# Kernel tuning notes

Measured on AMD Instinct MI355X. Metric: run time of the kernel, lower is better.

## Reference

```python
import jax, jax.numpy as jnp
import numpy as np

B, L1, L2, D = 32, 512, 512, 1024


def setup_inputs() -> dict:
    key = jax.random.key(0)
    k1, k2, k3, k4 = jax.random.split(key, 4)
    v1 = jax.random.normal(k1, (B, L1, D), dtype=jnp.float32)
    v2 = jax.random.normal(k2, (B, L2, D), dtype=jnp.float32)
    # row/column is fully masked (which would NaN the softmax).
    v1_mask = jax.random.uniform(k3, (B, L1)) < 0.2
    v2_mask = jax.random.uniform(k4, (B, L2)) < 0.2
    return {"v1": v1, "v2": v2, "v1_mask": v1_mask, "v2_mask": v2_mask}


def reference(v1, v2, v1_mask, v2_mask):
    # similarity: [B, L1, L2]
    sim = jnp.einsum("bid,bjd->bij", v1, v2)
    neg_inf = jnp.float32(-jnp.inf)
    # softmax over v2 positions (dim=2), masking padded v2 columns
    v1_v2_attn = jax.nn.softmax(
        jnp.where(v2_mask[:, None, :], neg_inf, sim), axis=2)
    # softmax over v1 positions (dim=1), masking padded v1 rows
    v2_v1_attn = jax.nn.softmax(
        jnp.where(v1_mask[:, :, None], neg_inf, sim), axis=1)
    attended_v1 = jnp.einsum("bij,bjd->bid", v1_v2_attn, v2)  # [B,L1,D]
    attended_v2 = jnp.einsum("bij,bid->bjd", v2_v1_attn, v1)  # [B,L2,D]
    attended_v1 = jnp.where(v1_mask[:, :, None], 0.0, attended_v1)
    attended_v2 = jnp.where(v2_mask[:, :, None], 0.0, attended_v2)
    return attended_v1, attended_v2
```

## Files before the change

kernel.cpp:

```cpp
#include <hip/hip_runtime.h>
#include <stdint.h>


#define Bn 32
#define Ln 512
#define Dn 1024

typedef __attribute__((ext_vector_type(4))) float f32x4;
typedef __attribute__((ext_vector_type(4))) unsigned short u16x4;
typedef __attribute__((ext_vector_type(8))) unsigned short u16x8;
typedef __attribute__((ext_vector_type(8))) __bf16 bf16x8;

__device__ __forceinline__ unsigned short f2bf(float f) {
  unsigned int u = __float_as_uint(f);
  u += 0x7FFFu + ((u >> 16) & 1u);
  return (unsigned short)(u >> 16);
}

__device__ __forceinline__ void async_cp16(const void* g, void* l) {
  __builtin_amdgcn_global_load_lds(
      (__attribute__((address_space(1))) void*)(g),
      (__attribute__((address_space(3))) void*)(l), 16, 0, 0);
}

__global__ __launch_bounds__(256) void conv_split(
    const float* __restrict__ v1, const float* __restrict__ v2,
    unsigned short* __restrict__ v1t, unsigned short* __restrict__ v2t,
    unsigned short* __restrict__ v1h, unsigned short* __restrict__ v1l,
    unsigned short* __restrict__ v2h, unsigned short* __restrict__ v2l) {
  __shared__ float tile[64][65];
  const int z = blockIdx.z;
  const float* src = (z < Bn) ? v1 : v2;
  unsigned short* dt = (z < Bn) ? v1t : v2t;
  unsigned short* dh = (z < Bn) ? v1h : v2h;
  unsigned short* dl = (z < Bn) ? v1l : v2l;
  const int b = z & 31;
  const int d0 = blockIdx.x << 6;
  const int l0 = blockIdx.y << 6;
  const int tid = threadIdx.x;
  const size_t bo = (size_t)b * Ln * Dn;

  f32x4 xa[2], xb[2];
#pragma unroll
  for (int it = 0; it < 2; it++) {
    int lin = (it << 8) + tid;
    int l = lin >> 3;
    int d8 = (lin & 7) << 3;
    const float* sp = src + (size_t)(b * Ln + l0 + l) * Dn + d0 + d8;
    xa[it] = *(const f32x4*)sp;
    xb[it] = *(const f32x4*)(sp + 4);
  }
#pragma unroll
  for (int it = 0; it < 2; it++) {
    int lin = (it << 8) + tid;
    int l = lin >> 3;
    int d8 = (lin & 7) << 3;
    float xs[8] = {xa[it][0], xa[it][1], xa[it][2], xa[it][3],
                   xb[it][0], xb[it][1], xb[it][2], xb[it][3]};
    u16x8 h8, lo8;
#pragma unroll
    for (int e = 0; e < 8; e++) {
      tile[l][d8 + e] = xs[e];
      unsigned int u = __float_as_uint(xs[e]);
      h8[e] = (unsigned short)(u >> 16);
      float hf = __uint_as_float(u & 0xFFFF0000u);
      lo8[e] = (unsigned short)(__float_as_uint(xs[e] - hf) >> 16);
    }
    int gl = l0 + l;
    int sd = (d0 + d8) ^ (((gl >> 1) & 3) << 3);
    size_t off = bo + (size_t)gl * Dn + sd;
    *(u16x8*)(dh + off) = h8;
    *(u16x8*)(dl + off) = lo8;
  }
  __syncthreads();
#pragma unroll
  for (int it = 0; it < 4; it++) {
    int lin = (it << 8) + tid;
    int d = lin >> 4;
    int l4 = (lin & 15) << 2;
    u16x4 o;
    o[0] = f2bf(tile[l4][d]);     o[1] = f2bf(tile[l4 + 1][d]);
    o[2] = f2bf(tile[l4 + 2][d]); o[3] = f2bf(tile[l4 + 3][d]);
    *(u16x4*)(dt + (size_t)(b * Dn + d0 + d) * Ln + l0 + l4) = o;
  }
}

__global__ __launch_bounds__(256) void sim_gemm(
    const unsigned short* __restrict__ Ahg, const unsigned short* __restrict__ Alg,
    const unsigned short* __restrict__ Bhg, const unsigned short* __restrict__ Blg,
    float* __restrict__ C, const int* __restrict__ v1m,
    const int* __restrict__ v2m,
    float* __restrict__ pmaxR, float* __restrict__ psumR,
    float* __restrict__ pmaxC, float* __restrict__ psumC) {
  __shared__ unsigned short sAh[2][4096], sAl[2][4096];
  __shared__ unsigned short sBh[2][4096], sBl[2][4096];
  const int bid = blockIdx.x;
  const int id = ((bid & 7) << 6) + (bid >> 3);
  const int b = id >> 4;
  const int m0 = ((id >> 2) & 3) << 7;
  const int n0 = (id & 3) << 7;
  const int tid = threadIdx.x;
  const int lane = tid & 63;
  const int wave = tid >> 6;
  const int wrow = (wave >> 1) << 6;
  const int wcol = (wave & 1) << 6;
  const int r = lane & 15;
  const int q = lane >> 4;
  const int srow = tid >> 2;
  const int skof = (tid & 3) << 3;
  const size_t bo = (size_t)b * Ln * Dn;
  const unsigned short* gah = Ahg + bo + (size_t)(m0 + srow) * Dn + skof;
  const unsigned short* gal = Alg + bo + (size_t)(m0 + srow) * Dn + skof;
  const unsigned short* gbh = Bhg + bo + (size_t)(n0 + srow) * Dn + skof;
  const unsigned short* gbl = Blg + bo + (size_t)(n0 + srow) * Dn + skof;
  const int ldsw = wave << 9;

#define SIM_STAGE(nb, kk)                                        \
  do {                                                           \
    async_cp16(gah + (kk), &sAh[nb][ldsw]);                      \
    async_cp16(gah + 64 * Dn + (kk), &sAh[nb][2048 + ldsw]);     \
    async_cp16(gal + (kk), &sAl[nb][ldsw]);                      \
    async_cp16(gal + 64 * Dn + (kk), &sAl[nb][2048 + ldsw]);     \
    async_cp16(gbh + (kk), &sBh[nb][ldsw]);                      \
    async_cp16(gbh + 64 * Dn + (kk), &sBh[nb][2048 + ldsw]);     \
    async_cp16(gbl + (kk), &sBl[nb][ldsw]);                      \
    async_cp16(gbl + 64 * Dn + (kk), &sBl[nb][2048 + ldsw]);     \
  } while (0)

  const f32x4 zero4 = {0.f, 0.f, 0.f, 0.f};
  f32x4 acc[4][4];
#pragma unroll
  for (int i = 0; i < 4; i++)
#pragma unroll
    for (int j = 0; j < 4; j++) acc[i][j] = zero4;

  SIM_STAGE(0, 0);
  __syncthreads();

  int cb = 0;
  for (int k0 = 0; k0 < Dn; k0 += 32, cb ^= 1) {
    if (k0 + 32 < Dn) SIM_STAGE(cb ^ 1, k0 + 32);
    bf16x8 ah[4], al[4], bh[4], bl[4];
#pragma unroll
    for (int t = 0; t < 4; t++) {
      int ra = wrow + (t << 4) + r;
      int sa = (ra << 5) + ((q ^ ((ra >> 1) & 3)) << 3);
      ah[t] = *(const bf16x8*)(&sAh[cb][sa]);
      al[t] = *(const bf16x8*)(&sAl[cb][sa]);
      int rb = wcol + (t << 4) + r;
      int sb = (rb << 5) + ((q ^ ((rb >> 1) & 3)) << 3);
      bh[t] = *(const bf16x8*)(&sBh[cb][sb]);
      bl[t] = *(const bf16x8*)(&sBl[cb][sb]);
    }
#pragma unroll
    for (int tm = 0; tm < 4; tm++)
#pragma unroll
      for (int tn = 0; tn < 4; tn++) {
        acc[tm][tn] = __builtin_amdgcn_mfma_f32_16x16x32_bf16(
            ah[tm], bh[tn], acc[tm][tn], 0, 0, 0);
        acc[tm][tn] = __builtin_amdgcn_mfma_f32_16x16x32_bf16(
            ah[tm], bl[tn], acc[tm][tn], 0, 0, 0);
        acc[tm][tn] = __builtin_amdgcn_mfma_f32_16x16x32_bf16(
            al[tm], bh[tn], acc[tm][tn], 0, 0, 0);
      }
    __syncthreads();
  }
#undef SIM_STAGE

  float* Cb = C + (size_t)b * Ln * Ln;
#pragma unroll
  for (int tm = 0; tm < 4; tm++) {
    int rowb = m0 + wrow + (tm << 4) + (q << 2);
#pragma unroll
    for (int reg = 0; reg < 4; reg++) {
      int row = rowb + reg;
#pragma unroll
      for (int tn = 0; tn < 4; tn++) {
        int col = n0 + wcol + (tn << 4) + r;
        Cb[(size_t)row * Ln + col] = acc[tm][tn][reg];
      }
    }
  }

  const int* mkr = v1m + (b << 9);
  const int* mkc = v2m + (b << 9);
  const float NEGINF = -__builtin_inff();
  unsigned cmb = 0;
#pragma unroll
  for (int tn = 0; tn < 4; tn++)
    cmb |= (mkc[n0 + wcol + (tn << 4) + r] ? 1u : 0u) << tn;
  unsigned rmb = 0;
#pragma unroll
  for (int t2 = 0; t2 < 16; t2++)
    rmb |= (mkr[m0 + wrow + ((t2 >> 2) << 4) + (q << 2) + (t2 & 3)] ? 1u : 0u)
           << t2;

  const int nsub = (n0 + wcol) >> 6;
#pragma unroll
  for (int tm = 0; tm < 4; tm++) {
#pragma unroll
    for (int reg = 0; reg < 4; reg++) {
      float m = NEGINF;
#pragma unroll
      for (int tn = 0; tn < 4; tn++)
        if (!((cmb >> tn) & 1)) m = fmaxf(m, acc[tm][tn][reg]);
#pragma unroll
      for (int off = 1; off < 16; off <<= 1)
        m = fmaxf(m, __shfl_xor(m, off));
      float s = 0.f;
#pragma unroll
      for (int tn = 0; tn < 4; tn++)
        if (!((cmb >> tn) & 1)) s += __expf(acc[tm][tn][reg] - m);
#pragma unroll
      for (int off = 1; off < 16; off <<= 1) s += __shfl_xor(s, off);
      if (r == 0) {
        int row = m0 + wrow + (tm << 4) + (q << 2) + reg;
        int idx = (((b << 3) + nsub) << 9) + row;
        pmaxR[idx] = m;
        psumR[idx] = s;
      }
    }
  }

  const int msub = (m0 + wrow) >> 6;
#pragma unroll
  for (int tn = 0; tn < 4; tn++) {
    float m = NEGINF;
#pragma unroll
    for (int tm = 0; tm < 4; tm++)
#pragma unroll
      for (int reg = 0; reg < 4; reg++)
        if (!((rmb >> ((tm << 2) + reg)) & 1))
          m = fmaxf(m, acc[tm][tn][reg]);
    m = fmaxf(m, __shfl_xor(m, 16));
    m = fmaxf(m, __shfl_xor(m, 32));
    float s = 0.f;
#pragma unroll
    for (int tm = 0; tm < 4; tm++)
#pragma unroll
      for (int reg = 0; reg < 4; reg++)
        if (!((rmb >> ((tm << 2) + reg)) & 1))
          s += __expf(acc[tm][tn][reg] - m);
    s += __shfl_xor(s, 16);
    s += __shfl_xor(s, 32);
    if (q == 0) {
      int col = n0 + wcol + (tn << 4) + r;
      int idx = (((b << 3) + msub) << 9) + col;
      pmaxC[idx] = m;
      psumC[idx] = s;
    }
  }
}

__global__ __launch_bounds__(256) void comb(
    const float* __restrict__ pmaxR, const float* __restrict__ psumR,
    const float* __restrict__ pmaxC, const float* __restrict__ psumC,
    float* __restrict__ rowmax, float* __restrict__ rowrs,
    float* __restrict__ colmax, float* __restrict__ colrs) {
  const int id = (blockIdx.x << 8) + threadIdx.x;
  const int side = id >> 14;
  const int x = id & 16383;
  const float* pm = side ? pmaxC : pmaxR;
  const float* ps = side ? psumC : psumR;
  const int bq = x >> 9;
  const int j = x & 511;
  const float NEGINF = -__builtin_inff();
  float mm[8], sv[8];
#pragma unroll
  for (int p = 0; p < 8; p++) {
    int idx = (((bq << 3) + p) << 9) + j;
    mm[p] = pm[idx];
    sv[p] = ps[idx];
  }
  float M = NEGINF;
#pragma unroll
  for (int p = 0; p < 8; p++) M = fmaxf(M, mm[p]);
  float S = 0.f;
#pragma unroll
  for (int p = 0; p < 8; p++)
    S += (mm[p] > NEGINF) ? sv[p] * __expf(mm[p] - M) : 0.f;
  float rs = 1.f / S;
  if (side) { colmax[x] = M; colrs[x] = rs; }
  else      { rowmax[x] = M; rowrs[x] = rs; }
}

__global__ __launch_bounds__(256) void norm_write(
    const float* __restrict__ sim, const int* __restrict__ v1m,
    const int* __restrict__ v2m,
    const float* __restrict__ rowmax, const float* __restrict__ rowrs,
    const float* __restrict__ colmax, const float* __restrict__ colrs,
    unsigned short* __restrict__ A1, unsigned short* __restrict__ A2t) {
  __shared__ unsigned short Tc[64][66];
  __shared__ float rm[64], rr[64], cmx[64], crx[64];
  __shared__ int jmk[64], imk[64];
  const int b = blockIdx.z;
  const int i0 = blockIdx.y << 6;
  const int j0 = blockIdx.x << 6;
  const int tid = threadIdx.x;
  if (tid < 64) {
    cmx[tid] = colmax[(b << 9) + j0 + tid];
    crx[tid] = colrs[(b << 9) + j0 + tid];
  } else if (tid < 128) {
    int t = tid - 64;
    rm[t] = rowmax[(b << 9) + i0 + t];
    rr[t] = rowrs[(b << 9) + i0 + t];
  } else if (tid < 192) {
    jmk[tid - 128] = v2m[(b << 9) + j0 + tid - 128];
  } else {
    imk[tid - 192] = v1m[(b << 9) + i0 + tid - 192];
  }
  __syncthreads();
  const int ri = tid >> 4;
  const int jj = (tid & 15) << 2;
  const float* Sb = sim + (size_t)b * (Ln * Ln);
  unsigned short* A1b = A1 + ((size_t)((b << 9) + i0)) * Ln + j0;
#pragma unroll
  for (int p = 0; p < 4; p++) {
    int il = (p << 4) + ri;
    f32x4 x = *(const f32x4*)(Sb + (size_t)(i0 + il) * Ln + j0 + jj);
    float rmv = rm[il], rrv = rr[il];
    int mrow = imk[il];
    u16x4 o1;
#pragma unroll
    for (int e = 0; e < 4; e++) {
      float e1 = jmk[jj + e] ? 0.f : __expf(x[e] - rmv) * rrv;
      o1[e] = f2bf(e1);
      float e2 = mrow ? 0.f : __expf(x[e] - cmx[jj + e]) * crx[jj + e];
      Tc[jj + e][il] = f2bf(e2);
    }
    *(u16x4*)(A1b + (size_t)il * Ln + jj) = o1;
  }
  __syncthreads();
  unsigned short* o = A2t + ((size_t)((b << 9) + j0)) * Ln + i0;
#pragma unroll
  for (int t = 0; t < 4; t++) {
    int c = (t << 8) + tid;
    int j = c >> 4;
    int ch = c & 15;
    u16x4 v;
    v[0] = Tc[j][(ch << 2)];     v[1] = Tc[j][(ch << 2) + 1];
    v[2] = Tc[j][(ch << 2) + 2]; v[3] = Tc[j][(ch << 2) + 3];
    *(u16x4*)(o + (size_t)j * Ln + (ch << 2)) = v;
  }
}

__global__ __launch_bounds__(256) void gemm_nt2(
    const unsigned short* __restrict__ A1g, const unsigned short* __restrict__ A2tg,
    const unsigned short* __restrict__ v2t, const unsigned short* __restrict__ v1t,
    float* __restrict__ out1, float* __restrict__ out2,
    const int* __restrict__ v1m, const int* __restrict__ v2m) {
  const int Mv = 512, Nv = 1024, Kv = 512;
  __shared__ unsigned short As[2][4096];
  __shared__ unsigned short Bs[2][4096];
  const int bid = blockIdx.x;
  const int id = ((bid & 7) << 8) + (bid >> 3);
  const int z = id >> 5;
  const int m0 = ((id >> 3) & 3) << 7;
  const int n0 = (id & 7) << 7;
  const int b = z & 31;
  const int w2 = z >> 5;
  const unsigned short* A = w2 ? A2tg : A1g;
  const unsigned short* Bm = w2 ? v1t : v2t;
  float* C = w2 ? out2 : out1;
  const int* rowmask = w2 ? v2m : v1m;
  const unsigned short* Ab = A + (size_t)b * Mv * Kv;
  const unsigned short* Bb = Bm + (size_t)b * Nv * Kv;
  float* Cb = C + (size_t)b * Mv * Nv;
  const int tid = threadIdx.x;
  const int lane = tid & 63;
  const int wave = tid >> 6;
  const int wrow = (wave >> 1) << 6;
  const int wcol = (wave & 1) << 6;

  const int srow = tid >> 2;
  const int skof = (tid & 3) << 3;
  const unsigned short* ga0 = Ab + (size_t)(m0 + srow) * Kv + skof;
  const unsigned short* ga1 = Ab + (size_t)(m0 + 64 + srow) * Kv + skof;
  const unsigned short* gb0 = Bb + (size_t)(n0 + srow) * Kv + skof;
  const unsigned short* gb1 = Bb + (size_t)(n0 + 64 + srow) * Kv + skof;
  const int ldsw = wave << 9;

#define PV_STAGE(nb, kk)                            \
  do {                                              \
    async_cp16(ga0 + (kk), &As[nb][ldsw]);          \
    async_cp16(ga1 + (kk), &As[nb][2048 + ldsw]);   \
    async_cp16(gb0 + (kk), &Bs[nb][ldsw]);          \
    async_cp16(gb1 + (kk), &Bs[nb][2048 + ldsw]);   \
  } while (0)

  const int r = lane & 15;
  const int q = lane >> 4;

  const f32x4 zero4 = {0.f, 0.f, 0.f, 0.f};
  f32x4 acc[4][4];
#pragma unroll
  for (int i = 0; i < 4; i++)
#pragma unroll
    for (int j = 0; j < 4; j++) acc[i][j] = zero4;

  PV_STAGE(0, 0);
  __syncthreads();

  int cb = 0;
  for (int k0 = 0; k0 < Kv; k0 += 32, cb ^= 1) {
    if (k0 + 32 < Kv) PV_STAGE(cb ^ 1, k0 + 32);
    bf16x8 af[4], bfr[4];
#pragma unroll
    for (int t = 0; t < 4; t++) {
      af[t] = *(const bf16x8*)(&As[cb][((wrow + (t << 4) + r) << 5) + (q << 3)]);
      bfr[t] = *(const bf16x8*)(&Bs[cb][((wcol + (t << 4) + r) << 5) + (q << 3)]);
    }
#pragma unroll
    for (int tm = 0; tm < 4; tm++)
#pragma unroll
      for (int tn = 0; tn < 4; tn++)
        acc[tm][tn] = __builtin_amdgcn_mfma_f32_16x16x32_bf16(
            af[tm], bfr[tn], acc[tm][tn], 0, 0, 0);
    __syncthreads();
  }
#undef PV_STAGE

  const int* mb = rowmask + b * Mv;
#pragma unroll
  for (int tm = 0; tm < 4; tm++) {
    int rowb = m0 + wrow + (tm << 4) + (q << 2);
#pragma unroll
    for (int reg = 0; reg < 4; reg++) {
      int row = rowb + reg;
      float mz = mb[row] ? 0.f : 1.f;
#pragma unroll
      for (int tn = 0; tn < 4; tn++) {
        int col = n0 + wcol + (tn << 4) + r;
        Cb[(size_t)row * Nv + col] = acc[tm][tn][reg] * mz;
      }
    }
  }
}

extern "C" void kernel_launch(void* const* d_in, const int* in_sizes, int n_in,
                              void* d_out, int out_size, void* d_ws,
                              size_t ws_size, hipStream_t stream) {
  (void)in_sizes; (void)n_in; (void)out_size; (void)ws_size;
  const float* v1 = (const float*)d_in[0];
  const float* v2 = (const float*)d_in[1];
  const int* v1m = (const int*)d_in[2];
  const int* v2m = (const int*)d_in[3];
  float* out1 = (float*)d_out;
  float* out2 = out1 + (size_t)Bn * Ln * Dn;

  char* ws = (char*)d_ws;
  const size_t Mi = 1048576;
  unsigned short* v1t = (unsigned short*)(ws);
  unsigned short* v2t = (unsigned short*)(ws + 32 * Mi);
  unsigned short* v1h = (unsigned short*)(ws + 64 * Mi);
  unsigned short* v2h = (unsigned short*)(ws + 96 * Mi);
  unsigned short* v1l = (unsigned short*)(ws + 128 * Mi);
  unsigned short* v2l = (unsigned short*)(ws + 160 * Mi);
  float* sim = (float*)(ws + 192 * Mi);
  unsigned short* A1 = (unsigned short*)(ws + 64 * Mi);
  unsigned short* A2t = (unsigned short*)(ws + 80 * Mi);
  float* pmaxR = (float*)(ws + 224 * Mi);
  float* psumR = (float*)(ws + 224 * Mi + 512 * 1024);
  float* pmaxC = (float*)(ws + 225 * Mi);
  float* psumC = (float*)(ws + 225 * Mi + 512 * 1024);
  float* rowmax = (float*)(ws + 226 * Mi);
  float* rowrs = (float*)(ws + 226 * Mi + 64 * 1024);
  float* colmax = (float*)(ws + 226 * Mi + 128 * 1024);
  float* colrs = (float*)(ws + 226 * Mi + 192 * 1024);

  dim3 blk(256);
  conv_split<<<dim3(16, 8, 64), blk, 0, stream>>>(v1, v2, v1t, v2t,
                                                  v1h, v1l, v2h, v2l);
  sim_gemm<<<dim3(512), blk, 0, stream>>>(v1h, v1l, v2h, v2l, sim,
                                          v1m, v2m, pmaxR, psumR,
                                          pmaxC, psumC);
  comb<<<dim3(128), blk, 0, stream>>>(pmaxR, psumR, pmaxC, psumC,
                                      rowmax, rowrs, colmax, colrs);
  norm_write<<<dim3(8, 8, 32), blk, 0, stream>>>(sim, v1m, v2m, rowmax, rowrs,
                                                 colmax, colrs, A1, A2t);
  gemm_nt2<<<dim3(2048), blk, 0, stream>>>(A1, A2t, v2t, v1t,
                                           out1, out2, v1m, v2m);
}
```

Before: 412.5 us.

## Fuse bf16 hi/lo split into sim GEMM and enlarge its tile to 256x256

The similarity GEMM now reads fp32 inputs directly and splits them into bf16 high/low parts in registers before writing to LDS. This removes the separate split pass and the hi/lo workspace traffic. The GEMM tile also grows from 128x128 with 256 threads to 256x256 with 512 threads, giving 128 blocks, and the column partial-stat reduction and combine kernel are resized to match. In exchange it drops the async double-buffered global-to-LDS copies for register-staged single-buffer loads with two barriers per k-step. With only 128 blocks, fewer than the number of CUs, part of the GPU may sit idle.

Measured after the change: 404.9 us. Within noise of the previous version (-1.8%).

```diff
diff --git a/kernel.cpp b/kernel.cpp
--- a/kernel.cpp
+++ b/kernel.cpp
@@ -23,54 +23,40 @@
       (__attribute__((address_space(3))) void*)(l), 16, 0, 0);
 }
 
-__global__ __launch_bounds__(256) void conv_split(
+__device__ __forceinline__ void split8(f32x4 x0, f32x4 x1,
+                                       u16x8* h, u16x8* l) {
+  float xs[8] = {x0[0], x0[1], x0[2], x0[3], x1[0], x1[1], x1[2], x1[3]};
+  u16x8 hh, ll;
+#pragma unroll
+  for (int e = 0; e < 8; e++) {
+    unsigned int u = __float_as_uint(xs[e]);
+    hh[e] = (unsigned short)(u >> 16);
+    float hf = __uint_as_float(u & 0xFFFF0000u);
+    ll[e] = (unsigned short)(__float_as_uint(xs[e] - hf) >> 16);
+  }
+  *h = hh;
+  *l = ll;
+}
+
+__global__ __launch_bounds__(256) void conv_t(
     const float* __restrict__ v1, const float* __restrict__ v2,
-    unsigned short* __restrict__ v1t, unsigned short* __restrict__ v2t,
-    unsigned short* __restrict__ v1h, unsigned short* __restrict__ v1l,
-    unsigned short* __restrict__ v2h, unsigned short* __restrict__ v2l) {
+    unsigned short* __restrict__ v1t, unsigned short* __restrict__ v2t) {
   __shared__ float tile[64][65];
   const int z = blockIdx.z;
   const float* src = (z < Bn) ? v1 : v2;
   unsigned short* dt = (z < Bn) ? v1t : v2t;
-  unsigned short* dh = (z < Bn) ? v1h : v2h;
-  unsigned short* dl = (z < Bn) ? v1l : v2l;
   const int b = z & 31;
   const int d0 = blockIdx.x << 6;
   const int l0 = blockIdx.y << 6;
   const int tid = threadIdx.x;
-  const size_t bo = (size_t)b * Ln * Dn;
-
-  f32x4 xa[2], xb[2];
-#pragma unroll
-  for (int it = 0; it < 2; it++) {
+#pragma unroll
+  for (int it = 0; it < 4; it++) {
     int lin = (it << 8) + tid;
-    int l = lin >> 3;
-    int d8 = (lin & 7) << 3;
-    const float* sp = src + (size_t)(b * Ln + l0 + l) * Dn + d0 + d8;
-    xa[it] = *(const f32x4*)sp;
-    xb[it] = *(const f32x4*)(sp + 4);
-  }
-#pragma unroll
-  for (int it = 0; it < 2; it++) {
-    int lin = (it << 8) + tid;
-    int l = lin >> 3;
-    int d8 = (lin & 7) << 3;
-    float xs[8] = {xa[it][0], xa[it][1], xa[it][2], xa[it][3],
-                   xb[it][0], xb[it][1], xb[it][2], xb[it][3]};
-    u16x8 h8, lo8;
-#pragma unroll
-    for (int e = 0; e < 8; e++) {
-      tile[l][d8 + e] = xs[e];
-      unsigned int u = __float_as_uint(xs[e]);
-      h8[e] = (unsigned short)(u >> 16);
-      float hf = __uint_as_float(u & 0xFFFF0000u);
-      lo8[e] = (unsigned short)(__float_as_uint(xs[e] - hf) >> 16);
-    }
-    int gl = l0 + l;
-    int sd = (d0 + d8) ^ (((gl >> 1) & 3) << 3);
-    size_t off = bo + (size_t)gl * Dn + sd;
-    *(u16x8*)(dh + off) = h8;
-    *(u16x8*)(dl + off) = lo8;
+    int l = lin >> 4;
+    int d4 = (lin & 15) << 2;
+    f32x4 x = *(const f32x4*)(src + (size_t)(b * Ln + l0 + l) * Dn + d0 + d4);
+    tile[l][d4] = x[0]; tile[l][d4 + 1] = x[1];
+    tile[l][d4 + 2] = x[2]; tile[l][d4 + 3] = x[3];
   }
   __syncthreads();
 #pragma unroll
@@ -85,98 +71,113 @@
   }
 }
 
-__global__ __launch_bounds__(256) void sim_gemm(
-    const unsigned short* __restrict__ Ahg, const unsigned short* __restrict__ Alg,
-    const unsigned short* __restrict__ Bhg, const unsigned short* __restrict__ Blg,
+__global__ __launch_bounds__(512) void sim_gemm(
+    const float* __restrict__ V1, const float* __restrict__ V2,
     float* __restrict__ C, const int* __restrict__ v1m,
     const int* __restrict__ v2m,
     float* __restrict__ pmaxR, float* __restrict__ psumR,
     float* __restrict__ pmaxC, float* __restrict__ psumC) {
-  __shared__ unsigned short sAh[2][4096], sAl[2][4096];
-  __shared__ unsigned short sBh[2][4096], sBl[2][4096];
+  __shared__ __align__(16) unsigned short sAh[8192], sAl[8192];
+  __shared__ __align__(16) unsigned short sBh[8192], sBl[8192];
   const int bid = blockIdx.x;
-  const int id = ((bid & 7) << 6) + (bid >> 3);
-  const int b = id >> 4;
-  const int m0 = ((id >> 2) & 3) << 7;
-  const int n0 = (id & 3) << 7;
+  const int id = ((bid & 7) << 4) + (bid >> 3);
+  const int b = id >> 2;
+  const int m0 = ((id >> 1) & 1) << 8;
+  const int n0 = (id & 1) << 8;
   const int tid = threadIdx.x;
   const int lane = tid & 63;
   const int wave = tid >> 6;
-  const int wrow = (wave >> 1) << 6;
-  const int wcol = (wave & 1) << 6;
+  const int wm = wave >> 2;
+  const int wn = wave & 3;
   const int r = lane & 15;
   const int q = lane >> 4;
-  const int srow = tid >> 2;
-  const int skof = (tid & 3) << 3;
+  const int srow = tid >> 1;
+  const int sc0 = (tid & 1) << 1;
+  const int ss = (srow >> 1) & 3;
   const size_t bo = (size_t)b * Ln * Dn;
-  const unsigned short* gah = Ahg + bo + (size_t)(m0 + srow) * Dn + skof;
-  const unsigned short* gal = Alg + bo + (size_t)(m0 + srow) * Dn + skof;
-  const unsigned short* gbh = Bhg + bo + (size_t)(n0 + srow) * Dn + skof;
-  const unsigned short* gbl = Blg + bo + (size_t)(n0 + srow) * Dn + skof;
-  const int ldsw = wave << 9;
-
-#define SIM_STAGE(nb, kk)                                        \
+  const float* gA = V1 + bo + (size_t)(m0 + srow) * Dn + (sc0 << 3);
+  const float* gB = V2 + bo + (size_t)(n0 + srow) * Dn + (sc0 << 3);
+  const int w0 = srow * 32 + ((sc0 ^ ss) << 3);
+  const int w1 = srow * 32 + (((sc0 + 1) ^ ss) << 3);
+
+  f32x4 xa[4], xb[4];
+#define SIM_LOAD(kk)                                             \
   do {                                                           \
-    async_cp16(gah + (kk), &sAh[nb][ldsw]);                      \
-    async_cp16(gah + 64 * Dn + (kk), &sAh[nb][2048 + ldsw]);     \
-    async_cp16(gal + (kk), &sAl[nb][ldsw]);                      \
-    async_cp16(gal + 64 * Dn + (kk), &sAl[nb][2048 + ldsw]);     \
-    async_cp16(gbh + (kk), &sBh[nb][ldsw]);                      \
-    async_cp16(gbh + 64 * Dn + (kk), &sBh[nb][2048 + ldsw]);     \
-    async_cp16(gbl + (kk), &sBl[nb][ldsw]);                      \
-    async_cp16(gbl + 64 * Dn + (kk), &sBl[nb][2048 + ldsw]);     \
+    const float* pa = gA + (kk);                                 \
+    const float* pb = gB + (kk);                                 \
+    xa[0] = *(const f32x4*)pa;       xa[1] = *(const f32x4*)(pa + 4);  \
+    xa[2] = *(const f32x4*)(pa + 8); xa[3] = *(const f32x4*)(pa + 12); \
+    xb[0] = *(const f32x4*)pb;       xb[1] = *(const f32x4*)(pb + 4);  \
+    xb[2] = *(const f32x4*)(pb + 8); xb[3] = *(const f32x4*)(pb + 12); \
   } while (0)
+#define SIM_CVTW()                                               \
+  do {                                                           \
+    u16x8 h_, l_;                                                \
+    split8(xa[0], xa[1], &h_, &l_);                              \
+    *(u16x8*)(sAh + w0) = h_; *(u16x8*)(sAl + w0) = l_;          \
+    split8(xa[2], xa[3], &h_, &l_);                              \
+    *(u16x8*)(sAh + w1) = h_; *(u16x8*)(sAl + w1) = l_;          \
+    split8(xb[0], xb[1], &h_, &l_);                              \
+    *(u16x8*)(sBh + w0) = h_; *(u16x8*)(sBl + w0) = l_;          \
+    split8(xb[2], xb[3], &h_, &l_);                              \
+    *(u16x8*)(sBh + w1) = h_; *(u16x8*)(sBl + w1) = l_;          \
+  } while (0)
 
   const f32x4 zero4 = {0.f, 0.f, 0.f, 0.f};
-  f32x4 acc[4][4];
-#pragma unroll
-  for (int i = 0; i < 4; i++)
+  f32x4 acc[8][4];
+#pragma unroll
+  for (int i = 0; i < 8; i++)
 #pragma unroll
     for (int j = 0; j < 4; j++) acc[i][j] = zero4;
 
-  SIM_STAGE(0, 0);
+  SIM_LOAD(0);
+  SIM_CVTW();
   __syncthreads();
 
-  int cb = 0;
-  for (int k0 = 0; k0 < Dn; k0 += 32, cb ^= 1) {
-    if (k0 + 32 < Dn) SIM_STAGE(cb ^ 1, k0 + 32);
-    bf16x8 ah[4], al[4], bh[4], bl[4];
-#pragma unroll
-    for (int t = 0; t < 4; t++) {
-      int ra = wrow + (t << 4) + r;
+  for (int k0 = 0; k0 < Dn; k0 += 32) {
+    const bool more = (k0 + 32 < Dn);
+    if (more) SIM_LOAD(k0 + 32);
+    bf16x8 bh[4], bl[4];
+#pragma unroll
+    for (int tn = 0; tn < 4; tn++) {
+      int rb = (wn << 6) + (tn << 4) + r;
+      int sb = (rb << 5) + ((q ^ ((rb >> 1) & 3)) << 3);
+      bh[tn] = *(const bf16x8*)(sBh + sb);
+      bl[tn] = *(const bf16x8*)(sBl + sb);
+    }
+#pragma unroll
+    for (int tm = 0; tm < 8; tm++) {
+      int ra = (wm << 7) + (tm << 4) + r;
       int sa = (ra << 5) + ((q ^ ((ra >> 1) & 3)) << 3);
-      ah[t] = *(const bf16x8*)(&sAh[cb][sa]);
-      al[t] = *(const bf16x8*)(&sAl[cb][sa]);
-      int rb = wcol + (t << 4) + r;
-      int sb = (rb << 5) + ((q ^ ((rb >> 1) & 3)) << 3);
-      bh[t] = *(const bf16x8*)(&sBh[cb][sb]);
-      bl[t] = *(const bf16x8*)(&sBl[cb][sb]);
-    }
-#pragma unroll
-    for (int tm = 0; tm < 4; tm++)
+      bf16x8 ah = *(const bf16x8*)(sAh + sa);
+      bf16x8 al = *(const bf16x8*)(sAl + sa);
 #pragma unroll
       for (int tn = 0; tn < 4; tn++) {
         acc[tm][tn] = __builtin_amdgcn_mfma_f32_16x16x32_bf16(
-            ah[tm], bh[tn], acc[tm][tn], 0, 0, 0);
+            ah, bh[tn], acc[tm][tn], 0, 0, 0);
         acc[tm][tn] = __builtin_amdgcn_mfma_f32_16x16x32_bf16(
-            ah[tm], bl[tn], acc[tm][tn], 0, 0, 0);
+            ah, bl[tn], acc[tm][tn], 0, 0, 0);
         acc[tm][tn] = __builtin_amdgcn_mfma_f32_16x16x32_bf16(
-            al[tm], bh[tn], acc[tm][tn], 0, 0, 0);
+            al, bh[tn], acc[tm][tn], 0, 0, 0);
       }
+    }
     __syncthreads();
-  }
-#undef SIM_STAGE
+    if (more) SIM_CVTW();
+    __syncthreads();
+  }
+#undef SIM_LOAD
+#undef SIM_CVTW
 
   float* Cb = C + (size_t)b * Ln * Ln;
 #pragma unroll
-  for (int tm = 0; tm < 4; tm++) {
-    int rowb = m0 + wrow + (tm << 4) + (q << 2);
+  for (int tm = 0; tm < 8; tm++) {
+    int rowb = m0 + (wm << 7) + (tm << 4) + (q << 2);
 #pragma unroll
     for (int reg = 0; reg < 4; reg++) {
       int row = rowb + reg;
 #pragma unroll
       for (int tn = 0; tn < 4; tn++) {
-        int col = n0 + wcol + (tn << 4) + r;
+        int col = n0 + (wn << 6) + (tn << 4) + r;
         Cb[(size_t)row * Ln + col] = acc[tm][tn][reg];
       }
     }
@@ -188,16 +189,16 @@
   unsigned cmb = 0;
 #pragma unroll
   for (int tn = 0; tn < 4; tn++)
-    cmb |= (mkc[n0 + wcol + (tn << 4) + r] ? 1u : 0u) << tn;
+    cmb |= (mkc[n0 + (wn << 6) + (tn << 4) + r] ? 1u : 0u) << tn;
   unsigned rmb = 0;
 #pragma unroll
-  for (int t2 = 0; t2 < 16; t2++)
-    rmb |= (mkr[m0 + wrow + ((t2 >> 2) << 4) + (q << 2) + (t2 & 3)] ? 1u : 0u)
-           << t2;
-
-  const int nsub = (n0 + wcol) >> 6;
-#pragma unroll
-  for (int tm = 0; tm < 4; tm++) {
+  for (int t2 = 0; t2 < 32; t2++)
+    rmb |= (mkr[m0 + (wm << 7) + ((t2 >> 2) << 4) + (q << 2) + (t2 & 3)]
+                ? 1u : 0u) << t2;
+
+  const int nsub = (n0 >> 6) + wn;
+#pragma unroll
+  for (int tm = 0; tm < 8; tm++) {
 #pragma unroll
     for (int reg = 0; reg < 4; reg++) {
       float m = NEGINF;
@@ -214,7 +215,7 @@
 #pragma unroll
       for (int off = 1; off < 16; off <<= 1) s += __shfl_xor(s, off);
       if (r == 0) {
-        int row = m0 + wrow + (tm << 4) + (q << 2) + reg;
+        int row = m0 + (wm << 7) + (tm << 4) + (q << 2) + reg;
         int idx = (((b << 3) + nsub) << 9) + row;
         pmaxR[idx] = m;
         psumR[idx] = s;
@@ -222,12 +223,12 @@
     }
   }
 
-  const int msub = (m0 + wrow) >> 6;
+  const int msub = (m0 >> 7) + wm;
 #pragma unroll
   for (int tn = 0; tn < 4; tn++) {
     float m = NEGINF;
 #pragma unroll
-    for (int tm = 0; tm < 4; tm++)
+    for (int tm = 0; tm < 8; tm++)
 #pragma unroll
       for (int reg = 0; reg < 4; reg++)
         if (!((rmb >> ((tm << 2) + reg)) & 1))
@@ -236,7 +237,7 @@
     m = fmaxf(m, __shfl_xor(m, 32));
     float s = 0.f;
 #pragma unroll
-    for (int tm = 0; tm < 4; tm++)
+    for (int tm = 0; tm < 8; tm++)
 #pragma unroll
       for (int reg = 0; reg < 4; reg++)
         if (!((rmb >> ((tm << 2) + reg)) & 1))
@@ -244,8 +245,8 @@
     s += __shfl_xor(s, 16);
     s += __shfl_xor(s, 32);
     if (q == 0) {
-      int col = n0 + wcol + (tn << 4) + r;
-      int idx = (((b << 3) + msub) << 9) + col;
+      int col = n0 + (wn << 6) + (tn << 4) + r;
+      int idx = (((b << 2) + msub) << 9) + col;
       pmaxC[idx] = m;
       psumC[idx] = s;
     }
@@ -260,28 +261,44 @@
   const int id = (blockIdx.x << 8) + threadIdx.x;
   const int side = id >> 14;
   const int x = id & 16383;
-  const float* pm = side ? pmaxC : pmaxR;
-  const float* ps = side ? psumC : psumR;
   const int bq = x >> 9;
   const int j = x & 511;
   const float NEGINF = -__builtin_inff();
-  float mm[8], sv[8];
-#pragma unroll
-  for (int p = 0; p < 8; p++) {
-    int idx = (((bq << 3) + p) << 9) + j;
-    mm[p] = pm[idx];
-    sv[p] = ps[idx];
-  }
-  float M = NEGINF;
-#pragma unroll
-  for (int p = 0; p < 8; p++) M = fmaxf(M, mm[p]);
-  float S = 0.f;
-#pragma unroll
-  for (int p = 0; p < 8; p++)
-    S += (mm[p] > NEGINF) ? sv[p] * __expf(mm[p] - M) : 0.f;
-  float rs = 1.f / S;
-  if (side) { colmax[x] = M; colrs[x] = rs; }
-  else      { rowmax[x] = M; rowrs[x] = rs; }
+  if (!side) {
+    float mm[8], sv[8];
+#pragma unroll
+    for (int p = 0; p < 8; p++) {
+      int idx = (((bq << 3) + p) << 9) + j;
+      mm[p] = pmaxR[idx];
+      sv[p] = psumR[idx];
+    }
+    float M = NEGINF;
+#pragma unroll
+    for (int p = 0; p < 8; p++) M = fmaxf(M, mm[p]);
+    float S = 0.f;
+#pragma unroll
+    for (int p = 0; p < 8; p++)
+      S += (mm[p] > NEGINF) ? sv[p] * __expf(mm[p] - M) : 0.f;
+    rowmax[x] = M;
+    rowrs[x] = 1.f / S;
+  } else {
+    float mm[4], sv[4];
+#pragma unroll
+    for (int p = 0; p < 4; p++) {
+      int idx = (((bq << 2) + p) << 9) + j;
+      mm[p] = pmaxC[idx];
+      sv[p] = psumC[idx];
+    }
+    float M = NEGINF;
+#pragma unroll
+    for (int p = 0; p < 4; p++) M = fmaxf(M, mm[p]);
+    float S = 0.f;
+#pragma unroll
+    for (int p = 0; p < 4; p++)
+      S += (mm[p] > NEGINF) ? sv[p] * __expf(mm[p] - M) : 0.f;
+    colmax[x] = M;
+    colrs[x] = 1.f / S;
+  }
 }
 
 __global__ __launch_bounds__(256) void norm_write(
@@ -452,28 +469,22 @@
   const size_t Mi = 1048576;
   unsigned short* v1t = (unsigned short*)(ws);
   unsigned short* v2t = (unsigned short*)(ws + 32 * Mi);
-  unsigned short* v1h = (unsigned short*)(ws + 64 * Mi);
-  unsigned short* v2h = (unsigned short*)(ws + 96 * Mi);
-  unsigned short* v1l = (unsigned short*)(ws + 128 * Mi);
-  unsigned short* v2l = (unsigned short*)(ws + 160 * Mi);
-  float* sim = (float*)(ws + 192 * Mi);
-  unsigned short* A1 = (unsigned short*)(ws + 64 * Mi);
-  unsigned short* A2t = (unsigned short*)(ws + 80 * Mi);
-  float* pmaxR = (float*)(ws + 224 * Mi);
-  float* psumR = (float*)(ws + 224 * Mi + 512 * 1024);
-  float* pmaxC = (float*)(ws + 225 * Mi);
-  float* psumC = (float*)(ws + 225 * Mi + 512 * 1024);
-  float* rowmax = (float*)(ws + 226 * Mi);
-  float* rowrs = (float*)(ws + 226 * Mi + 64 * 1024);
-  float* colmax = (float*)(ws + 226 * Mi + 128 * 1024);
-  float* colrs = (float*)(ws + 226 * Mi + 192 * 1024);
+  float* sim = (float*)(ws + 64 * Mi);
+  unsigned short* A1 = (unsigned short*)(ws + 96 * Mi);
+  unsigned short* A2t = (unsigned short*)(ws + 112 * Mi);
+  float* pmaxR = (float*)(ws + 128 * Mi);
+  float* psumR = (float*)(ws + 128 * Mi + 512 * 1024);
+  float* pmaxC = (float*)(ws + 129 * Mi);
+  float* psumC = (float*)(ws + 129 * Mi + 256 * 1024);
+  float* rowmax = (float*)(ws + 129 * Mi + 512 * 1024);
+  float* rowrs = (float*)(ws + 129 * Mi + 576 * 1024);
+  float* colmax = (float*)(ws + 129 * Mi + 640 * 1024);
+  float* colrs = (float*)(ws + 129 * Mi + 704 * 1024);
 
   dim3 blk(256);
-  conv_split<<<dim3(16, 8, 64), blk, 0, stream>>>(v1, v2, v1t, v2t,
-                                                  v1h, v1l, v2h, v2l);
-  sim_gemm<<<dim3(512), blk, 0, stream>>>(v1h, v1l, v2h, v2l, sim,
-                                          v1m, v2m, pmaxR, psumR,
-                                          pmaxC, psumC);
+  conv_t<<<dim3(16, 8, 64), blk, 0, stream>>>(v1, v2, v1t, v2t);
+  sim_gemm<<<dim3(128), dim3(512), 0, stream>>>(v1, v2, sim, v1m, v2m,
+                                                pmaxR, psumR, pmaxC, psumC);
   comb<<<dim3(128), blk, 0, stream>>>(pmaxR, psumR, pmaxC, psumC,
                                       rowmax, rowrs, colmax, colrs);
   norm_write<<<dim3(8, 8, 32), blk, 0, stream>>>(sim, v1m, v2m, rowmax, rowrs,
```
